# Kernel optimization log

Hardware: AMD Instinct MI355X
Metric: run time of the kernel (lower is better)

Reference implementation:

```python
import jax, jax.numpy as jnp
import numpy as np

NUM_EXPERTS = 8
TOP_K = 2

def setup_inputs() -> dict:
    key = jax.random.key(0)
    ks = jax.random.split(key, 6)
    B, S, D, H, E = 4, 2048, 1024, 4096, NUM_EXPERTS
    sc_g = 1.0 / np.sqrt(D)
    sc_1 = 1.0 / np.sqrt(D)
    sc_2 = 1.0 / np.sqrt(H)
    return {
        "x": jax.random.normal(ks[0], (B, S, D), dtype=jnp.float32),
        "Wg": jax.random.normal(ks[1], (D, E), dtype=jnp.float32) * sc_g,
        "W1": jax.random.normal(ks[2], (E, D, H), dtype=jnp.float32) * sc_1,
        "b1": jnp.zeros((E, H), dtype=jnp.float32),
        "W2": jax.random.normal(ks[3], (E, H, D), dtype=jnp.float32) * sc_2,
        "b2": jnp.zeros((E, D), dtype=jnp.float32),
    }

def reference(x, Wg, W1, b1, W2, b2):
    B, S, D = x.shape
    E = Wg.shape[1]
    T = B * S
    xf = x.reshape(T, D)

    # ---- Router (SparseRouter) ----
    logits = xf @ Wg                      # [T, E]
    probs = jax.nn.softmax(logits, axis=-1)
    w, idx = jax.lax.top_k(probs, TOP_K)  # [T, K]
    w = w / jnp.sum(w, axis=-1, keepdims=True)

    rows = jnp.arange(T)[:, None]
    # combine[t,e] = sum_k w[t,k] * 1[idx[t,k]==e]  (dispatch/combine weights)
    combine = jnp.zeros((T, E), dtype=xf.dtype).at[rows, idx].add(w)
    # load-balancing aux loss
    counts = jnp.zeros((T, E), dtype=xf.dtype).at[rows, idx].add(1.0)
    f_i = counts.mean(axis=0)
    p_i = probs.mean(axis=0)
    aux_loss = E * jnp.sum(f_i * p_i)

    # ---- Experts (ExpertFFN, dropout=identity in eval) ----
    h = jnp.einsum('td,edh->teh', xf, W1) + b1[None]      # [T, E, H]
    h = jax.nn.gelu(h, approximate=False)                  # torch GELU (exact erf)
    y = jnp.einsum('teh,ehd->ted', h, W2) + b2[None]       # [T, E, D]

    out = jnp.einsum('te,ted->td', combine, y).reshape(B, S, D)
    return (out, aux_loss)
```

## Files before the change

### kernel.cpp

```cpp
#include <hip/hip_runtime.h>
#include <hip/hip_bf16.h>
#include <math.h>

#define TTOK 8192
#define DDIM 1024
#define HDIM 4096
#define NEXP 8
#define BMT 256
#define MAXT 72
#define MAXSLOTS (MAXT * BMT)

typedef __bf16 bf16x8 __attribute__((ext_vector_type(8)));
typedef float f32x4 __attribute__((ext_vector_type(4)));
typedef const void __attribute__((address_space(1))) *gvp_t;
typedef void __attribute__((address_space(3))) *lvp_t;

__device__ __forceinline__ void gload16(const void *g, void *l) {
  __builtin_amdgcn_global_load_lds((gvp_t)g, (lvp_t)l, 16, 0, 0);
}
__device__ __forceinline__ void bar() {
  asm volatile("" ::: "memory");
  __builtin_amdgcn_s_barrier();
  asm volatile("" ::: "memory");
}
__device__ __forceinline__ void wait_lgkm0() {
  asm volatile("s_waitcnt lgkmcnt(0)" ::: "memory");
}
template <int N> __device__ __forceinline__ void wait_vm() {
  if constexpr (N == 0) asm volatile("s_waitcnt vmcnt(0)" ::: "memory");
  else if constexpr (N == 2) asm volatile("s_waitcnt vmcnt(2)" ::: "memory");
  else if constexpr (N == 4) asm volatile("s_waitcnt vmcnt(4)" ::: "memory");
  else if constexpr (N == 6) asm volatile("s_waitcnt vmcnt(6)" ::: "memory");
}


__global__ __launch_bounds__(64) void zero_meta(int *counts, int *cursors, float *probsum) {
  int i = threadIdx.x;
  if (i < NEXP) { counts[i] = 0; cursors[i] = 0; probsum[i] = 0.f; }
}

__global__ __launch_bounds__(256) void convert_x(const float *__restrict__ x,
                                                 __hip_bfloat16 *__restrict__ xb) {
  size_t i = ((size_t)blockIdx.x * 256 + threadIdx.x) * 4;
  float4 v = *(const float4 *)(x + i);
  union { __hip_bfloat16 h[4]; uint2 u; } p;
  p.h[0] = __float2bfloat16(v.x);
  p.h[1] = __float2bfloat16(v.y);
  p.h[2] = __float2bfloat16(v.z);
  p.h[3] = __float2bfloat16(v.w);
  *(uint2 *)(xb + i) = p.u;
}

__global__ __launch_bounds__(256) void transpose_cvt(const float *__restrict__ src,
                                                     __hip_bfloat16 *__restrict__ dst,
                                                     int R, int C) {
  __shared__ float tile[64][65];
  const int e = blockIdx.z;
  const int rb = blockIdx.x * 64, cb = blockIdx.y * 64;
  const size_t base = (size_t)e * R * C;
  const int lx = threadIdx.x & 63, ly = threadIdx.x >> 6;
#pragma unroll
  for (int i = 0; i < 64; i += 4)
    tile[ly + i][lx] = src[base + (size_t)(rb + ly + i) * C + cb + lx];
  __syncthreads();
#pragma unroll
  for (int i = 0; i < 64; i += 4)
    dst[base + (size_t)(cb + ly + i) * R + rb + lx] = __float2bfloat16(tile[lx][ly + i]);
}

__global__ __launch_bounds__(256) void router_k(const float *__restrict__ x,
                                                const float *__restrict__ Wg,
                                                int *__restrict__ counts,
                                                float *__restrict__ probsum,
                                                int *__restrict__ tok_e,
                                                float *__restrict__ tok_w) {
  __shared__ float sprob[NEXP];
  __shared__ int scnt[NEXP];
  if (threadIdx.x < NEXP) { sprob[threadIdx.x] = 0.f; scnt[threadIdx.x] = 0; }
  __syncthreads();

  const int wid = threadIdx.x >> 6, lane = threadIdx.x & 63;
  const int t = blockIdx.x * 4 + wid;
  const float *xr = x + (size_t)t * DDIM;
  double acc[NEXP];
#pragma unroll
  for (int e = 0; e < NEXP; ++e) acc[e] = 0.0;
  for (int j = lane; j < DDIM; j += 64) {
    double xv = (double)xr[j];
    const float *wrow = Wg + j * NEXP;
#pragma unroll
    for (int e = 0; e < NEXP; ++e) acc[e] += xv * (double)wrow[e];
  }
#pragma unroll
  for (int e = 0; e < NEXP; ++e) {
#pragma unroll
    for (int off = 32; off > 0; off >>= 1) acc[e] += __shfl_xor(acc[e], off, 64);
  }
  if (lane == 0) {
    double mx = acc[0];
    for (int e = 1; e < NEXP; ++e) mx = acc[e] > mx ? acc[e] : mx;
    double p[NEXP], s = 0.0;
    for (int e = 0; e < NEXP; ++e) { p[e] = exp(acc[e] - mx); s += p[e]; }
    for (int e = 0; e < NEXP; ++e) p[e] /= s;
    int i0 = 0;
    for (int e = 1; e < NEXP; ++e) if (p[e] > p[i0]) i0 = e;
    int i1 = (i0 == 0) ? 1 : 0;
    for (int e = 0; e < NEXP; ++e) if (e != i0 && p[e] > p[i1]) i1 = e;
    tok_e[t] = i0 | (i1 << 16);
    tok_w[t] = (float)(p[i0] / (p[i0] + p[i1]));
    atomicAdd(&scnt[i0], 1);
    atomicAdd(&scnt[i1], 1);
    for (int e = 0; e < NEXP; ++e) atomicAdd(&sprob[e], (float)p[e]);
  }
  __syncthreads();
  if (threadIdx.x < NEXP) {
    atomicAdd(&counts[threadIdx.x], scnt[threadIdx.x]);
    atomicAdd(&probsum[threadIdx.x], sprob[threadIdx.x]);
  }
}

__global__ __launch_bounds__(256) void offsets_k(const int *__restrict__ counts,
                                                 int *__restrict__ padoff,
                                                 int *__restrict__ tileexp,
                                                 int *__restrict__ total,
                                                 int *__restrict__ slot_tok,
                                                 float *__restrict__ slot_w) {
  __shared__ int sp[NEXP + 1];
  if (threadIdx.x == 0) {
    int off = 0, tt = 0;
    for (int e = 0; e < NEXP; ++e) {
      sp[e] = off;
      padoff[e] = off;
      int nt = (counts[e] + BMT - 1) >> 8;
      for (int i = 0; i < nt; ++i) tileexp[tt + i] = e;
      tt += nt;
      off += nt << 8;
    }
    sp[NEXP] = off;
    *total = tt;
  }
  __syncthreads();
  for (int e = 0; e < NEXP; ++e) {
    int s0 = sp[e] + counts[e], s1 = sp[e + 1];
    for (int s = s0 + (int)threadIdx.x; s < s1; s += 256) {
      slot_tok[s] = 0;
      slot_w[s] = 0.f;
    }
  }
}

__global__ __launch_bounds__(256) void assign_k(const int *__restrict__ tok_e,
                                                const float *__restrict__ tok_w,
                                                const int *__restrict__ padoff,
                                                int *__restrict__ cursors,
                                                int *__restrict__ slot_tok,
                                                float *__restrict__ slot_w,
                                                int *__restrict__ slot_of) {
  const int t = blockIdx.x * 256 + threadIdx.x;
  const int ee = tok_e[t];
  const int e0 = ee & 0xffff, e1 = ee >> 16;
  const float w0 = tok_w[t];
  int p0 = atomicAdd(&cursors[e0], 1);
  int s0 = padoff[e0] + p0;
  slot_tok[s0] = t; slot_w[s0] = w0; slot_of[2 * t] = s0;
  int p1 = atomicAdd(&cursors[e1], 1);
  int s1 = padoff[e1] + p1;
  slot_tok[s1] = t; slot_w[s1] = 1.0f - w0; slot_of[2 * t + 1] = s1;
}

template <int KDIM_, int NDIM_, bool GELU_, bool GATHER_>
__global__ __launch_bounds__(512, 2) void moe_gemm8(
    const __hip_bfloat16 *__restrict__ A, const __hip_bfloat16 *__restrict__ Bw,
    const float *__restrict__ bias, __hip_bfloat16 *__restrict__ Cout,
    const int *__restrict__ slot_token, const int *__restrict__ tile_expert,
    const int *__restrict__ total_tiles) {
  constexpr int BUFSZ = 49152;
  __shared__ __align__(16) char lds[2 * BUFSZ];

  const int tile = blockIdx.x;
  if (tile >= *total_tiles) return;
  const int e = tile_expert[tile];
  const int ncol = blockIdx.y * 128;
  const int tid = threadIdx.x, wid = tid >> 6, lane = tid & 63;

  const int sr = lane >> 3;
  const int scs = ((lane & 7) ^ sr) * 8;
  const __hip_bfloat16 *ap[2][2], *bp[2];
  const __hip_bfloat16 *Bb = Bw + (size_t)e * ((size_t)NDIM_ * KDIM_);
#pragma unroll
  for (int h = 0; h < 2; ++h)
#pragma unroll
    for (int g = 0; g < 2; ++g) {
      int r = tile * 256 + h * 128 + g * 64 + wid * 8 + sr;
      int row = GATHER_ ? slot_token[r] : r;
      ap[h][g] = A + (size_t)row * KDIM_ + scs;
    }
#pragma unroll
  for (int g = 0; g < 2; ++g)
    bp[g] = Bb + (size_t)(ncol + g * 64 + wid * 8 + sr) * KDIM_ + scs;

  const int woff = wid * 1024;
  const int wr = wid >> 2, wc = wid & 3;
  const int ln15 = lane & 15, g4 = lane >> 4, ln7 = lane & 7;
  int aoff[4], boff[2], coff[2];
#pragma unroll
  for (int m = 0; m < 4; ++m) aoff[m] = (wr * 64 + m * 16 + ln15) * 128;
#pragma unroll
  for (int n = 0; n < 2; ++n) boff[n] = 32768 + (wc * 32 + n * 16 + ln15) * 128;
#pragma unroll
  for (int kc = 0; kc < 2; ++kc) coff[kc] = ((kc * 4 + g4) ^ ln7) * 16;

  f32x4 acc[8][2] = {};
  constexpr int nkt = KDIM_ / 64;

  wait_vm<0>();
#pragma unroll
  for (int g = 0; g < 2; ++g) gload16(ap[0][g], lds + g * 8192 + woff);
#pragma unroll
  for (int g = 0; g < 2; ++g) gload16(bp[g], lds + 32768 + g * 8192 + woff);
#pragma unroll
  for (int g = 0; g < 2; ++g) gload16(ap[1][g], lds + 16384 + g * 8192 + woff);
  wait_vm<2>();
  bar();

  for (int kt = 0; kt < nkt; ++kt) {
    const bool last = (kt == nkt - 1);
    const int b = kt & 1;
    char *cb = lds + b * BUFSZ;
    char *ob = lds + (b ^ 1) * BUFSZ;

    bf16x8 af[4][2], bfr[2][2];
#pragma unroll
    for (int m = 0; m < 4; ++m)
#pragma unroll
      for (int kc = 0; kc < 2; ++kc)
        af[m][kc] = *(const bf16x8 *)(cb + aoff[m] + coff[kc]);
#pragma unroll
    for (int n = 0; n < 2; ++n)
#pragma unroll
      for (int kc = 0; kc < 2; ++kc)
        bfr[n][kc] = *(const bf16x8 *)(cb + boff[n] + coff[kc]);
    if (!last) {
#pragma unroll
      for (int g = 0; g < 2; ++g) gload16(ap[0][g] + (kt + 1) * 64, ob + g * 8192 + woff);
#pragma unroll
      for (int g = 0; g < 2; ++g) gload16(bp[g] + (kt + 1) * 64, ob + 32768 + g * 8192 + woff);
      wait_vm<4>();
    } else {
      wait_vm<0>();
    }
    bar();
    wait_lgkm0();
    __builtin_amdgcn_s_setprio(1);
#pragma unroll
    for (int m = 0; m < 4; ++m)
#pragma unroll
      for (int n = 0; n < 2; ++n) {
        acc[m][n] = __builtin_amdgcn_mfma_f32_16x16x32_bf16(af[m][0], bfr[n][0], acc[m][n], 0, 0, 0);
        acc[m][n] = __builtin_amdgcn_mfma_f32_16x16x32_bf16(af[m][1], bfr[n][1], acc[m][n], 0, 0, 0);
      }
    __builtin_amdgcn_s_setprio(0);
    bar();

#pragma unroll
    for (int m = 0; m < 4; ++m)
#pragma unroll
      for (int kc = 0; kc < 2; ++kc)
        af[m][kc] = *(const bf16x8 *)(cb + 16384 + aoff[m] + coff[kc]);
#pragma unroll
    for (int n = 0; n < 2; ++n)
#pragma unroll
      for (int kc = 0; kc < 2; ++kc)
        bfr[n][kc] = *(const bf16x8 *)(cb + boff[n] + coff[kc]);
    if (!last) {
#pragma unroll
      for (int g = 0; g < 2; ++g) gload16(ap[1][g] + (kt + 1) * 64, ob + 16384 + g * 8192 + woff);
      wait_vm<2>();
    }
    bar();
    wait_lgkm0();
    __builtin_amdgcn_s_setprio(1);
#pragma unroll
    for (int m = 0; m < 4; ++m)
#pragma unroll
      for (int n = 0; n < 2; ++n) {
        acc[4 + m][n] = __builtin_amdgcn_mfma_f32_16x16x32_bf16(af[m][0], bfr[n][0], acc[4 + m][n], 0, 0, 0);
        acc[4 + m][n] = __builtin_amdgcn_mfma_f32_16x16x32_bf16(af[m][1], bfr[n][1], acc[4 + m][n], 0, 0, 0);
      }
    __builtin_amdgcn_s_setprio(0);
    bar();
  }

  const float *be = bias + (size_t)e * NDIM_;
  const int cbase = ncol + wc * 32 + ln15;
  float bv[2];
  bv[0] = be[cbase];
  bv[1] = be[cbase + 16];
#pragma unroll
  for (int mi = 0; mi < 8; ++mi) {
    const int row = tile * 256 + (mi >> 2) * 128 + wr * 64 + (mi & 3) * 16 + g4 * 4;
#pragma unroll
    for (int n = 0; n < 2; ++n) {
      const int col = cbase + n * 16;
#pragma unroll
      for (int r = 0; r < 4; ++r) {
        float v = acc[mi][n][r] + bv[n];
        if constexpr (GELU_) v = 0.5f * v * (1.0f + erff(v * 0.70710678118654752f));
        Cout[(size_t)(row + r) * NDIM_ + col] = __float2bfloat16(v);
      }
    }
  }
}

__global__ __launch_bounds__(256) void combine_k(const __hip_bfloat16 *__restrict__ yb,
                                                 const int *__restrict__ slot_of,
                                                 const float *__restrict__ slot_w,
                                                 float *__restrict__ out) {
  const int t = blockIdx.x;
  const int s0 = slot_of[2 * t], s1 = slot_of[2 * t + 1];
  const float w0 = slot_w[s0], w1 = slot_w[s1];
  const unsigned short *y = (const unsigned short *)yb;
  const int c = threadIdx.x * 4;
  ushort4 a = *(const ushort4 *)(y + (size_t)s0 * DDIM + c);
  ushort4 b = *(const ushort4 *)(y + (size_t)s1 * DDIM + c);
  float4 r;
  r.x = w0 * __uint_as_float((unsigned)a.x << 16) + w1 * __uint_as_float((unsigned)b.x << 16);
  r.y = w0 * __uint_as_float((unsigned)a.y << 16) + w1 * __uint_as_float((unsigned)b.y << 16);
  r.z = w0 * __uint_as_float((unsigned)a.z << 16) + w1 * __uint_as_float((unsigned)b.z << 16);
  r.w = w0 * __uint_as_float((unsigned)a.w << 16) + w1 * __uint_as_float((unsigned)b.w << 16);
  *(float4 *)(out + (size_t)t * DDIM + c) = r;
}

__global__ __launch_bounds__(64) void aux_k(const int *__restrict__ counts,
                                            const float *__restrict__ probsum,
                                            float *__restrict__ outp) {
  if (threadIdx.x == 0) {
    double s = 0.0;
    for (int e = 0; e < NEXP; ++e)
      s += ((double)counts[e] / (double)TTOK) * ((double)probsum[e] / (double)TTOK);
    *outp = (float)((double)NEXP * s);
  }
}

extern "C" void kernel_launch(void *const *d_in, const int *in_sizes, int n_in,
                              void *d_out, int out_size, void *d_ws, size_t ws_size,
                              hipStream_t stream) {
  const float *x  = (const float *)d_in[0];
  const float *Wg = (const float *)d_in[1];
  const float *W1 = (const float *)d_in[2];
  const float *b1 = (const float *)d_in[3];
  const float *W2 = (const float *)d_in[4];
  const float *b2 = (const float *)d_in[5];
  float *out = (float *)d_out;

  char *ws = (char *)d_ws;
  const size_t MB = 1ull << 20;
  int   *counts   = (int *)(ws + 0);
  int   *cursors  = (int *)(ws + 64);
  int   *padoff   = (int *)(ws + 128);
  int   *tileexp  = (int *)(ws + 192);
  int   *total    = (int *)(ws + 768);
  float *probsum  = (float *)(ws + 832);
  int   *tok_e    = (int *)(ws + 4096);
  float *tok_w    = (float *)(ws + 36864);
  int   *slot_tok = (int *)(ws + 69632);
  float *slot_w   = (float *)(ws + 147456);
  int   *slot_of  = (int *)(ws + 225280);
  __hip_bfloat16 *xb  = (__hip_bfloat16 *)(ws + 1 * MB);
  __hip_bfloat16 *w1t = (__hip_bfloat16 *)(ws + 17 * MB);
  __hip_bfloat16 *hb  = (__hip_bfloat16 *)(ws + 81 * MB);
  __hip_bfloat16 *w2t = (__hip_bfloat16 *)(ws + 1 * MB);
  __hip_bfloat16 *yb  = (__hip_bfloat16 *)(ws + 225 * MB);

  zero_meta<<<1, 64, 0, stream>>>(counts, cursors, probsum);
  convert_x<<<8192, 256, 0, stream>>>(x, xb);
  transpose_cvt<<<dim3(16, 64, 8), 256, 0, stream>>>(W1, w1t, DDIM, HDIM);
  router_k<<<TTOK / 4, 256, 0, stream>>>(x, Wg, counts, probsum, tok_e, tok_w);
  offsets_k<<<1, 256, 0, stream>>>(counts, padoff, tileexp, total, slot_tok, slot_w);
  assign_k<<<TTOK / 256, 256, 0, stream>>>(tok_e, tok_w, padoff, cursors, slot_tok, slot_w, slot_of);
  moe_gemm8<DDIM, HDIM, true, true><<<dim3(MAXT, HDIM / 128), 512, 0, stream>>>(
      xb, w1t, b1, hb, slot_tok, tileexp, total);
  transpose_cvt<<<dim3(64, 16, 8), 256, 0, stream>>>(W2, w2t, HDIM, DDIM);
  moe_gemm8<HDIM, DDIM, false, false><<<dim3(MAXT, DDIM / 128), 512, 0, stream>>>(
      hb, w2t, b2, yb, slot_tok, tileexp, total);
  combine_k<<<TTOK, 256, 0, stream>>>(yb, slot_of, slot_w, out);
  aux_k<<<1, 64, 0, stream>>>(counts, probsum, out + (size_t)TTOK * DDIM);
}
```

Measured before the change: 682.4 us.

## Restructure MoE GEMM with templated tile width and simpler double-buffered pipeline

The expert GEMM kernel gains template parameters for block N width and the wave-row layout. GEMM1 now uses 256x256 tiles with 2x4 waves, each computing a 128x64 sub-tile, while GEMM2 keeps 256x128 tiles with 4x2 waves of 64x64. The K-loop swaps the split half-tile staging scheme for a plain double buffer that issues the full next stage after one vmcnt(0) and barrier, then runs MFMA phases that reuse B fragments across more A rows. This raises per-wave reuse and cuts barrier and wait bookkeeping. In exchange GEMM1 needs more LDS and accumulator registers, and it launches fewer blocks, which may hurt occupancy.

After: 766.8 us. 12.4% more time.

```diff
diff --git a/kernel.cpp b/kernel.cpp
--- a/kernel.cpp
+++ b/kernel.cpp
@@ -17,20 +17,6 @@
 
 __device__ __forceinline__ void gload16(const void *g, void *l) {
   __builtin_amdgcn_global_load_lds((gvp_t)g, (lvp_t)l, 16, 0, 0);
-}
-__device__ __forceinline__ void bar() {
-  asm volatile("" ::: "memory");
-  __builtin_amdgcn_s_barrier();
-  asm volatile("" ::: "memory");
-}
-__device__ __forceinline__ void wait_lgkm0() {
-  asm volatile("s_waitcnt lgkmcnt(0)" ::: "memory");
-}
-template <int N> __device__ __forceinline__ void wait_vm() {
-  if constexpr (N == 0) asm volatile("s_waitcnt vmcnt(0)" ::: "memory");
-  else if constexpr (N == 2) asm volatile("s_waitcnt vmcnt(2)" ::: "memory");
-  else if constexpr (N == 4) asm volatile("s_waitcnt vmcnt(4)" ::: "memory");
-  else if constexpr (N == 6) asm volatile("s_waitcnt vmcnt(6)" ::: "memory");
 }
 
 
@@ -168,145 +154,116 @@
   slot_tok[s1] = t; slot_w[s1] = 1.0f - w0; slot_of[2 * t + 1] = s1;
 }
 
-template <int KDIM_, int NDIM_, bool GELU_, bool GATHER_>
+template <int KDIM_, int NDIM_, int BN_, int WRW_, bool GELU_, bool GATHER_>
 __global__ __launch_bounds__(512, 2) void moe_gemm8(
     const __hip_bfloat16 *__restrict__ A, const __hip_bfloat16 *__restrict__ Bw,
     const float *__restrict__ bias, __hip_bfloat16 *__restrict__ Cout,
     const int *__restrict__ slot_token, const int *__restrict__ tile_expert,
     const int *__restrict__ total_tiles) {
-  constexpr int BUFSZ = 49152;
-  __shared__ __align__(16) char lds[2 * BUFSZ];
+  constexpr int WCW = 8 / WRW_;
+  constexpr int PWM = 256 / WRW_;
+  constexpr int MF = PWM / 16;
+  constexpr int NBL = BN_ / 64;
+  constexpr int ABUF = 32768;
+  constexpr int BBUF = BN_ * 128;
+  static_assert(BN_ / WCW == 64, "per-wave N must be 64");
+
+  __shared__ __align__(16) char lsA[2 * ABUF];
+  __shared__ __align__(16) char lsB[2 * BBUF];
 
   const int tile = blockIdx.x;
   if (tile >= *total_tiles) return;
   const int e = tile_expert[tile];
-  const int ncol = blockIdx.y * 128;
+  const int ncol = blockIdx.y * BN_;
   const int tid = threadIdx.x, wid = tid >> 6, lane = tid & 63;
 
   const int sr = lane >> 3;
   const int scs = ((lane & 7) ^ sr) * 8;
-  const __hip_bfloat16 *ap[2][2], *bp[2];
   const __hip_bfloat16 *Bb = Bw + (size_t)e * ((size_t)NDIM_ * KDIM_);
-#pragma unroll
-  for (int h = 0; h < 2; ++h)
-#pragma unroll
-    for (int g = 0; g < 2; ++g) {
-      int r = tile * 256 + h * 128 + g * 64 + wid * 8 + sr;
-      int row = GATHER_ ? slot_token[r] : r;
-      ap[h][g] = A + (size_t)row * KDIM_ + scs;
+  const __hip_bfloat16 *ap[4], *bp[NBL];
+#pragma unroll
+  for (int c = 0; c < 4; ++c) {
+    int r = tile * 256 + c * 64 + wid * 8 + sr;
+    int row = GATHER_ ? slot_token[r] : r;
+    ap[c] = A + (size_t)row * KDIM_ + scs;
+  }
+#pragma unroll
+  for (int c = 0; c < NBL; ++c)
+    bp[c] = Bb + (size_t)(ncol + c * 64 + wid * 8 + sr) * KDIM_ + scs;
+  const int sdst = wid * 1024;
+
+  const int wr = wid / WCW, wc = wid % WCW;
+  const int ln15 = lane & 15, g4 = lane >> 4;
+  int abase[2], bbase[2];
+#pragma unroll
+  for (int kc = 0; kc < 2; ++kc) {
+    const int xsl = ((kc * 4 + g4) ^ (ln15 & 7)) << 4;
+    abase[kc] = (wr * PWM + ln15) * 128 + xsl;
+    bbase[kc] = (wc * 64 + ln15) * 128 + xsl;
+  }
+
+  f32x4 acc[MF][4] = {};
+  constexpr int nkt = KDIM_ / 64;
+
+  auto STAGE = [&](int buf, int kt) {
+#pragma unroll
+    for (int c = 0; c < 4; ++c)
+      gload16(ap[c] + kt * 64, lsA + buf * ABUF + c * 8192 + sdst);
+#pragma unroll
+    for (int c = 0; c < NBL; ++c)
+      gload16(bp[c] + kt * 64, lsB + buf * BBUF + c * 8192 + sdst);
+  };
+
+  STAGE(0, 0);
+  for (int kt = 0; kt < nkt; ++kt) {
+    const int b = kt & 1;
+    asm volatile("s_waitcnt vmcnt(0)" ::: "memory");
+    __builtin_amdgcn_s_barrier();
+    if (kt + 1 < nkt) STAGE(b ^ 1, kt + 1);
+    bf16x8 bfr[4][2];
+#pragma unroll
+    for (int ni = 0; ni < 4; ++ni)
+#pragma unroll
+      for (int kc = 0; kc < 2; ++kc)
+        bfr[ni][kc] = *(const bf16x8 *)(lsB + b * BBUF + bbase[kc] + ni * 2048);
+#pragma unroll
+    for (int ph = 0; ph < (MF / 4) * 2; ++ph) {
+      const int mh = (MF == 8) ? (ph & 1) : 0;
+      const int kc = (MF == 8) ? (ph >> 1) : ph;
+      bf16x8 af[4];
+#pragma unroll
+      for (int m = 0; m < 4; ++m)
+        af[m] = *(const bf16x8 *)(lsA + b * ABUF + abase[kc] + (mh * 4 + m) * 2048);
+      asm volatile("s_waitcnt lgkmcnt(0)" ::: "memory");
+      __builtin_amdgcn_sched_barrier(0);
+      __builtin_amdgcn_s_setprio(1);
+#pragma unroll
+      for (int m = 0; m < 4; ++m)
+#pragma unroll
+        for (int n = 0; n < 4; ++n)
+          acc[mh * 4 + m][n] = __builtin_amdgcn_mfma_f32_16x16x32_bf16(
+              af[m], bfr[n][kc], acc[mh * 4 + m][n], 0, 0, 0);
+      __builtin_amdgcn_s_setprio(0);
+      __builtin_amdgcn_s_barrier();
     }
-#pragma unroll
-  for (int g = 0; g < 2; ++g)
-    bp[g] = Bb + (size_t)(ncol + g * 64 + wid * 8 + sr) * KDIM_ + scs;
-
-  const int woff = wid * 1024;
-  const int wr = wid >> 2, wc = wid & 3;
-  const int ln15 = lane & 15, g4 = lane >> 4, ln7 = lane & 7;
-  int aoff[4], boff[2], coff[2];
-#pragma unroll
-  for (int m = 0; m < 4; ++m) aoff[m] = (wr * 64 + m * 16 + ln15) * 128;
-#pragma unroll
-  for (int n = 0; n < 2; ++n) boff[n] = 32768 + (wc * 32 + n * 16 + ln15) * 128;
-#pragma unroll
-  for (int kc = 0; kc < 2; ++kc) coff[kc] = ((kc * 4 + g4) ^ ln7) * 16;
-
-  f32x4 acc[8][2] = {};
-  constexpr int nkt = KDIM_ / 64;
-
-  wait_vm<0>();
-#pragma unroll
-  for (int g = 0; g < 2; ++g) gload16(ap[0][g], lds + g * 8192 + woff);
-#pragma unroll
-  for (int g = 0; g < 2; ++g) gload16(bp[g], lds + 32768 + g * 8192 + woff);
-#pragma unroll
-  for (int g = 0; g < 2; ++g) gload16(ap[1][g], lds + 16384 + g * 8192 + woff);
-  wait_vm<2>();
-  bar();
-
-  for (int kt = 0; kt < nkt; ++kt) {
-    const bool last = (kt == nkt - 1);
-    const int b = kt & 1;
-    char *cb = lds + b * BUFSZ;
-    char *ob = lds + (b ^ 1) * BUFSZ;
-
-    bf16x8 af[4][2], bfr[2][2];
-#pragma unroll
-    for (int m = 0; m < 4; ++m)
-#pragma unroll
-      for (int kc = 0; kc < 2; ++kc)
-        af[m][kc] = *(const bf16x8 *)(cb + aoff[m] + coff[kc]);
-#pragma unroll
-    for (int n = 0; n < 2; ++n)
-#pragma unroll
-      for (int kc = 0; kc < 2; ++kc)
-        bfr[n][kc] = *(const bf16x8 *)(cb + boff[n] + coff[kc]);
-    if (!last) {
-#pragma unroll
-      for (int g = 0; g < 2; ++g) gload16(ap[0][g] + (kt + 1) * 64, ob + g * 8192 + woff);
-#pragma unroll
-      for (int g = 0; g < 2; ++g) gload16(bp[g] + (kt + 1) * 64, ob + 32768 + g * 8192 + woff);
-      wait_vm<4>();
-    } else {
-      wait_vm<0>();
-    }
-    bar();
-    wait_lgkm0();
-    __builtin_amdgcn_s_setprio(1);
-#pragma unroll
-    for (int m = 0; m < 4; ++m)
-#pragma unroll
-      for (int n = 0; n < 2; ++n) {
-        acc[m][n] = __builtin_amdgcn_mfma_f32_16x16x32_bf16(af[m][0], bfr[n][0], acc[m][n], 0, 0, 0);
-        acc[m][n] = __builtin_amdgcn_mfma_f32_16x16x32_bf16(af[m][1], bfr[n][1], acc[m][n], 0, 0, 0);
-      }
-    __builtin_amdgcn_s_setprio(0);
-    bar();
-
-#pragma unroll
-    for (int m = 0; m < 4; ++m)
-#pragma unroll
-      for (int kc = 0; kc < 2; ++kc)
-        af[m][kc] = *(const bf16x8 *)(cb + 16384 + aoff[m] + coff[kc]);
-#pragma unroll
-    for (int n = 0; n < 2; ++n)
-#pragma unroll
-      for (int kc = 0; kc < 2; ++kc)
-        bfr[n][kc] = *(const bf16x8 *)(cb + boff[n] + coff[kc]);
-    if (!last) {
-#pragma unroll
-      for (int g = 0; g < 2; ++g) gload16(ap[1][g] + (kt + 1) * 64, ob + 16384 + g * 8192 + woff);
-      wait_vm<2>();
-    }
-    bar();
-    wait_lgkm0();
-    __builtin_amdgcn_s_setprio(1);
-#pragma unroll
-    for (int m = 0; m < 4; ++m)
-#pragma unroll
-      for (int n = 0; n < 2; ++n) {
-        acc[4 + m][n] = __builtin_amdgcn_mfma_f32_16x16x32_bf16(af[m][0], bfr[n][0], acc[4 + m][n], 0, 0, 0);
-        acc[4 + m][n] = __builtin_amdgcn_mfma_f32_16x16x32_bf16(af[m][1], bfr[n][1], acc[4 + m][n], 0, 0, 0);
-      }
-    __builtin_amdgcn_s_setprio(0);
-    bar();
   }
 
   const float *be = bias + (size_t)e * NDIM_;
-  const int cbase = ncol + wc * 32 + ln15;
-  float bv[2];
-  bv[0] = be[cbase];
-  bv[1] = be[cbase + 16];
-#pragma unroll
-  for (int mi = 0; mi < 8; ++mi) {
-    const int row = tile * 256 + (mi >> 2) * 128 + wr * 64 + (mi & 3) * 16 + g4 * 4;
-#pragma unroll
-    for (int n = 0; n < 2; ++n) {
-      const int col = cbase + n * 16;
+  const int colb = ncol + wc * 64 + ln15;
+  float bv[4];
+#pragma unroll
+  for (int ni = 0; ni < 4; ++ni) bv[ni] = be[colb + ni * 16];
+#pragma unroll
+  for (int mi = 0; mi < MF; ++mi) {
+    const int row0 = tile * 256 + wr * PWM + mi * 16 + g4 * 4;
+#pragma unroll
+    for (int ni = 0; ni < 4; ++ni) {
+      const int col = colb + ni * 16;
 #pragma unroll
       for (int r = 0; r < 4; ++r) {
-        float v = acc[mi][n][r] + bv[n];
+        float v = acc[mi][ni][r] + bv[ni];
         if constexpr (GELU_) v = 0.5f * v * (1.0f + erff(v * 0.70710678118654752f));
-        Cout[(size_t)(row + r) * NDIM_ + col] = __float2bfloat16(v);
+        Cout[(size_t)(row0 + r) * NDIM_ + col] = __float2bfloat16(v);
       }
     }
   }
@@ -378,10 +335,10 @@
   router_k<<<TTOK / 4, 256, 0, stream>>>(x, Wg, counts, probsum, tok_e, tok_w);
   offsets_k<<<1, 256, 0, stream>>>(counts, padoff, tileexp, total, slot_tok, slot_w);
   assign_k<<<TTOK / 256, 256, 0, stream>>>(tok_e, tok_w, padoff, cursors, slot_tok, slot_w, slot_of);
-  moe_gemm8<DDIM, HDIM, true, true><<<dim3(MAXT, HDIM / 128), 512, 0, stream>>>(
+  moe_gemm8<DDIM, HDIM, 256, 2, true, true><<<dim3(MAXT, HDIM / 256), 512, 0, stream>>>(
       xb, w1t, b1, hb, slot_tok, tileexp, total);
   transpose_cvt<<<dim3(64, 16, 8), 256, 0, stream>>>(W2, w2t, HDIM, DDIM);
-  moe_gemm8<HDIM, DDIM, false, false><<<dim3(MAXT, DDIM / 128), 512, 0, stream>>>(
+  moe_gemm8<HDIM, DDIM, 128, 4, false, false><<<dim3(MAXT, DDIM / 128), 512, 0, stream>>>(
       hb, w2t, b2, yb, slot_tok, tileexp, total);
   combine_k<<<TTOK, 256, 0, stream>>>(yb, slot_of, slot_w, out);
   aux_k<<<1, 64, 0, stream>>>(counts, probsum, out + (size_t)TTOK * DDIM);
```
